# Kernel optimization log

Hardware: AMD Instinct MI355X
Metric: run time of the kernel (lower is better)

## Reference

```python
import jax, jax.numpy as jnp
import numpy as np

SAMPLING_RATE = 0.5

def setup_inputs() -> dict:
    key = jax.random.key(0)
    k1, k2 = jax.random.split(key)
    token = jax.random.normal(k1, (8, 16, 4, 384), dtype=jnp.float32)
    feature = jax.random.normal(k2, (8, 16, 4, 196, 384), dtype=jnp.float32)
    return {"token": token, "feature": feature}

def reference(token, feature):
    b1, n1, kk1, c = token.shape
    b2, n2, kk2, hw, _ = feature.shape
    N = n1 * kk1  # == n2 * kk2
    tok = token.reshape(b1, N, 1, c)           # [b, N, 1, c]
    feat = feature.reshape(b2, N, hw, c)       # [b, N, hw, c]
    scale = c ** (-0.5)
    # attention scores: [b, N, 1, hw]
    attn = jnp.einsum('bnqc,bnhc->bnqh', tok, feat) * scale
    attn = jax.nn.softmax(attn, axis=-1)
    tk = int(hw * SAMPLING_RATE)
    sel_attn, sel_idx = jax.lax.top_k(attn, tk)          # [b, N, 1, tk]
    sel_attn = sel_attn / jnp.sum(sel_attn, axis=-1, keepdims=True)
    # gather selected features: idx [b, N, tk] -> feat rows [b, N, tk, c]
    idx = sel_idx[:, :, 0, :]                            # [b, N, tk]
    sel_feat = jnp.take_along_axis(feat, idx[..., None], axis=2)  # [b, N, tk, c]
    out = jnp.einsum('bnqt,bntc->bnqc', sel_attn, sel_feat)       # [b, N, 1, c]
    return out.reshape(b1, n1, kk1, c)
```

## Files before the change

### kernel.cpp

```cpp
#include <hip/hip_runtime.h>
#include <hip/hip_fp16.h>

#define HW 196
#define C  384
#define CF4 (C/4)
#define TK 98
#define NT 512
#define NWAVE (NT/64)

__global__ __launch_bounds__(NT, 4) void sampling_kernel(
    const float* __restrict__ token,
    const float* __restrict__ feature,
    float* __restrict__ out)
{
    __shared__ __align__(16) unsigned char stash_raw[TK * C * 2];
    __shared__ float tokLds[C];
    __shared__ float score[HW];
    __shared__ float selW[TK];
    __shared__ int   selIdx[TK];
    __shared__ float wsum[NWAVE];
    __shared__ int   rank2[2 * HW];
    __shared__ float s_max, s_winv;

    __half (*feat16)[C] = (__half(*)[C])stash_raw;
    float  (*part)[C]   = (float(*)[C])stash_raw;

    const int tid  = threadIdx.x;
    const int wave = tid >> 6;
    const int lane = tid & 63;
    const int l8   = lane & 7;
    const int g8   = lane >> 3;
    const int pair = blockIdx.x;

    const float* tokp  = token   + (size_t)pair * C;
    const float* featp = feature + (size_t)pair * (HW * C);
    const float4* f4base = (const float4*)featp;
    const float4* t4     = (const float4*)tokLds;

    for (int i = tid; i < C; i += NT) tokLds[i] = tokp[i];
    __syncthreads();

    float4 tok[12];
    #pragma unroll
    for (int k = 0; k < 12; ++k) tok[k] = t4[l8 + 8 * k];

    const float scale = 0.05103103630798288f;

    #pragma unroll
    for (int it = 0; it < 3; ++it) {
        const int r = it * 64 + wave * 8 + g8;
        const float4* fr = f4base + (size_t)r * CF4 + l8;
        float4 a[12];
        #pragma unroll
        for (int k = 0; k < 12; ++k) a[k] = fr[8 * k];
        float4 acc = make_float4(0.f, 0.f, 0.f, 0.f);
        #pragma unroll
        for (int k = 0; k < 12; ++k) {
            acc.x += a[k].x * tok[k].x; acc.y += a[k].y * tok[k].y;
            acc.z += a[k].z * tok[k].z; acc.w += a[k].w * tok[k].w;
        }
        if (r < TK) {
            #pragma unroll
            for (int k = 0; k < 12; ++k) {
                union { uint2 u; __half2 h[2]; } W;
                W.h[0] = __floats2half2_rn(a[k].x, a[k].y);
                W.h[1] = __floats2half2_rn(a[k].z, a[k].w);
                *(uint2*)&feat16[r][4 * l8 + 32 * k] = W.u;
            }
        }
        float s = (acc.x + acc.y) + (acc.z + acc.w);
        s += __shfl_xor(s, 1, 64);
        s += __shfl_xor(s, 2, 64);
        s += __shfl_xor(s, 4, 64);
        if (l8 == 0) score[r] = s * scale;
    }
    if (wave < 4 && g8 == 0) {
        const int r = 192 + wave;
        const float4* fr = f4base + (size_t)r * CF4 + l8;
        float4 acc = make_float4(0.f, 0.f, 0.f, 0.f);
        #pragma unroll
        for (int k = 0; k < 12; ++k) {
            float4 a = fr[8 * k];
            acc.x += a.x * tok[k].x; acc.y += a.y * tok[k].y;
            acc.z += a.z * tok[k].z; acc.w += a.w * tok[k].w;
        }
        float s = (acc.x + acc.y) + (acc.z + acc.w);
        s += __shfl_xor(s, 1, 64);
        s += __shfl_xor(s, 2, 64);
        s += __shfl_xor(s, 4, 64);
        if (l8 == 0) score[r] = s * scale;
    }
    __syncthreads();

    if (tid < 2 * HW) {
        const int i = tid >> 1, h = tid & 1;
        const float si = score[i];
        int cnt = 0;
        const int j0 = h * (HW / 2);
        for (int j = j0; j < j0 + HW / 2; ++j) {
            const float sj = score[j];
            cnt += (int)((sj > si) | ((sj == si) & (j < i)));
        }
        rank2[tid] = cnt;
    } else if (wave == NWAVE - 1) {
        float m = -3.4e38f;
        for (int i = lane; i < HW; i += 64) m = fmaxf(m, score[i]);
        #pragma unroll
        for (int off = 32; off > 0; off >>= 1)
            m = fmaxf(m, __shfl_xor(m, off, 64));
        if (lane == 0) s_max = m;
    }
    __syncthreads();

    float w = 0.f;
    if (tid < HW) {
        const int rank = rank2[2 * tid] + rank2[2 * tid + 1];
        if (rank < TK) {
            w = __expf(score[tid] - s_max);
            selIdx[rank] = tid;
            selW[rank]  = w;
        }
    }
    #pragma unroll
    for (int off = 32; off > 0; off >>= 1) w += __shfl_xor(w, off, 64);
    if (lane == 0) wsum[wave] = w;
    __syncthreads();
    if (tid == 0) {
        float s = 0.f;
        #pragma unroll
        for (int i = 0; i < NWAVE; ++i) s += wsum[i];
        s_winv = 1.f / s;
    }
    __syncthreads();

    float4 acc_a = make_float4(0.f, 0.f, 0.f, 0.f);
    float4 acc_b = make_float4(0.f, 0.f, 0.f, 0.f);
    #pragma unroll
    for (int j = 0; j < 13; ++j) {
        const int i = wave + NWAVE * j;
        if (i < TK) {
            const int   r   = selIdx[i];
            const float wgt = selW[i];
            if (r < TK) {
                union { uint2 u; __half2 h[2]; } U;
                U.u = *(const uint2*)&feat16[r][4 * lane];
                float2 f0 = __half22float2(U.h[0]);
                float2 f1 = __half22float2(U.h[1]);
                acc_a.x += wgt * f0.x; acc_a.y += wgt * f0.y;
                acc_a.z += wgt * f1.x; acc_a.w += wgt * f1.y;
                if (lane < 32) {
                    union { uint2 u; __half2 h[2]; } V;
                    V.u = *(const uint2*)&feat16[r][256 + 4 * lane];
                    float2 g0 = __half22float2(V.h[0]);
                    float2 g1 = __half22float2(V.h[1]);
                    acc_b.x += wgt * g0.x; acc_b.y += wgt * g0.y;
                    acc_b.z += wgt * g1.x; acc_b.w += wgt * g1.y;
                }
            } else {
                const float4* f4 = f4base + (size_t)r * CF4;
                float4 aa = f4[lane];
                acc_a.x += wgt * aa.x; acc_a.y += wgt * aa.y;
                acc_a.z += wgt * aa.z; acc_a.w += wgt * aa.w;
                if (lane < 32) {
                    float4 bb = f4[64 + lane];
                    acc_b.x += wgt * bb.x; acc_b.y += wgt * bb.y;
                    acc_b.z += wgt * bb.z; acc_b.w += wgt * bb.w;
                }
            }
        }
    }
    __syncthreads();

    float4* pw = (float4*)&part[wave][0];
    pw[lane] = acc_a;
    if (lane < 32) pw[64 + lane] = acc_b;
    __syncthreads();

    if (tid < C) {
        float s = 0.f;
        #pragma unroll
        for (int wv = 0; wv < NWAVE; ++wv) s += part[wv][tid];
        out[(size_t)pair * C + tid] = s * s_winv;
    }
}

extern "C" void kernel_launch(void* const* d_in, const int* in_sizes, int n_in,
                              void* d_out, int out_size, void* d_ws, size_t ws_size,
                              hipStream_t stream) {
    const float* token   = (const float*)d_in[0];
    const float* feature = (const float*)d_in[1];
    float* out = (float*)d_out;
    const int pairs = in_sizes[0] / C;
    sampling_kernel<<<pairs, NT, 0, stream>>>(token, feature, out);
}
```

Baseline: 36.87 us.

## Keep first 128 feature rows in registers as fp16, stash rest in LDS

The kernel no longer re-reads unstashed selected rows from global memory. Rows 0-127 are now held in registers as fp16 and accumulated with per-row weights (zero when not selected) plus cross-lane shuffle reductions. The remaining 68 rows are stashed in LDS with a padded stride. This removes the second global gather for rows 98-195 and the separate top-k gather for low rows, at the cost of more registers, shuffle work and extra LDS (separate part buffer), which may reduce occupancy.

```diff
diff --git a/kernel.cpp b/kernel.cpp
--- a/kernel.cpp
+++ b/kernel.cpp
@@ -7,23 +7,24 @@
 #define TK 98
 #define NT 512
 #define NWAVE (NT/64)
+#define RSTRIDE 400
+#define NSTASH 68
 
 __global__ __launch_bounds__(NT, 4) void sampling_kernel(
     const float* __restrict__ token,
     const float* __restrict__ feature,
     float* __restrict__ out)
 {
-    __shared__ __align__(16) unsigned char stash_raw[TK * C * 2];
+    __shared__ __half stash[NSTASH * RSTRIDE];
     __shared__ float tokLds[C];
     __shared__ float score[HW];
+    __shared__ float wFlag[128];
     __shared__ float selW[TK];
     __shared__ int   selIdx[TK];
+    __shared__ int   rank2[2 * HW];
     __shared__ float wsum[NWAVE];
-    __shared__ int   rank2[2 * HW];
+    __shared__ float part[NWAVE][C];
     __shared__ float s_max, s_winv;
-
-    __half (*feat16)[C] = (__half(*)[C])stash_raw;
-    float  (*part)[C]   = (float(*)[C])stash_raw;
 
     const int tid  = threadIdx.x;
     const int wave = tid >> 6;
@@ -32,22 +33,19 @@
     const int g8   = lane >> 3;
     const int pair = blockIdx.x;
 
-    const float* tokp  = token   + (size_t)pair * C;
-    const float* featp = feature + (size_t)pair * (HW * C);
-    const float4* f4base = (const float4*)featp;
-    const float4* t4     = (const float4*)tokLds;
+    const float* tokp = token + (size_t)pair * C;
+    const float4* f4base = (const float4*)(feature + (size_t)pair * (HW * C));
+    const float4* t4 = (const float4*)tokLds;
 
     for (int i = tid; i < C; i += NT) tokLds[i] = tokp[i];
     __syncthreads();
 
-    float4 tok[12];
+    const float scale = 0.05103103630798288f;
+
+    uint2 r16[2][12];
+
     #pragma unroll
-    for (int k = 0; k < 12; ++k) tok[k] = t4[l8 + 8 * k];
-
-    const float scale = 0.05103103630798288f;
-
-    #pragma unroll
-    for (int it = 0; it < 3; ++it) {
+    for (int it = 0; it < 2; ++it) {
         const int r = it * 64 + wave * 8 + g8;
         const float4* fr = f4base + (size_t)r * CF4 + l8;
         float4 a[12];
@@ -56,17 +54,13 @@
         float4 acc = make_float4(0.f, 0.f, 0.f, 0.f);
         #pragma unroll
         for (int k = 0; k < 12; ++k) {
-            acc.x += a[k].x * tok[k].x; acc.y += a[k].y * tok[k].y;
-            acc.z += a[k].z * tok[k].z; acc.w += a[k].w * tok[k].w;
-        }
-        if (r < TK) {
-            #pragma unroll
-            for (int k = 0; k < 12; ++k) {
-                union { uint2 u; __half2 h[2]; } W;
-                W.h[0] = __floats2half2_rn(a[k].x, a[k].y);
-                W.h[1] = __floats2half2_rn(a[k].z, a[k].w);
-                *(uint2*)&feat16[r][4 * l8 + 32 * k] = W.u;
-            }
+            float4 t = t4[l8 + 8 * k];
+            acc.x += a[k].x * t.x; acc.y += a[k].y * t.y;
+            acc.z += a[k].z * t.z; acc.w += a[k].w * t.w;
+            union { uint2 u; __half2 h[2]; } W;
+            W.h[0] = __floats2half2_rn(a[k].x, a[k].y);
+            W.h[1] = __floats2half2_rn(a[k].z, a[k].w);
+            r16[it][k] = W.u;
         }
         float s = (acc.x + acc.y) + (acc.z + acc.w);
         s += __shfl_xor(s, 1, 64);
@@ -74,15 +68,46 @@
         s += __shfl_xor(s, 4, 64);
         if (l8 == 0) score[r] = s * scale;
     }
+
+    {
+        const int r = 128 + wave * 8 + g8;
+        const float4* fr = f4base + (size_t)r * CF4 + l8;
+        __half* srow = &stash[(r - 128) * RSTRIDE];
+        float4 a[12];
+        #pragma unroll
+        for (int k = 0; k < 12; ++k) a[k] = fr[8 * k];
+        float4 acc = make_float4(0.f, 0.f, 0.f, 0.f);
+        #pragma unroll
+        for (int k = 0; k < 12; ++k) {
+            float4 t = t4[l8 + 8 * k];
+            acc.x += a[k].x * t.x; acc.y += a[k].y * t.y;
+            acc.z += a[k].z * t.z; acc.w += a[k].w * t.w;
+            union { uint2 u; __half2 h[2]; } W;
+            W.h[0] = __floats2half2_rn(a[k].x, a[k].y);
+            W.h[1] = __floats2half2_rn(a[k].z, a[k].w);
+            *(uint2*)&srow[4 * l8 + 32 * k] = W.u;
+        }
+        float s = (acc.x + acc.y) + (acc.z + acc.w);
+        s += __shfl_xor(s, 1, 64);
+        s += __shfl_xor(s, 2, 64);
+        s += __shfl_xor(s, 4, 64);
+        if (l8 == 0) score[r] = s * scale;
+    }
     if (wave < 4 && g8 == 0) {
         const int r = 192 + wave;
         const float4* fr = f4base + (size_t)r * CF4 + l8;
+        __half* srow = &stash[(r - 128) * RSTRIDE];
         float4 acc = make_float4(0.f, 0.f, 0.f, 0.f);
         #pragma unroll
         for (int k = 0; k < 12; ++k) {
             float4 a = fr[8 * k];
-            acc.x += a.x * tok[k].x; acc.y += a.y * tok[k].y;
-            acc.z += a.z * tok[k].z; acc.w += a.w * tok[k].w;
+            float4 t = t4[l8 + 8 * k];
+            acc.x += a.x * t.x; acc.y += a.y * t.y;
+            acc.z += a.z * t.z; acc.w += a.w * t.w;
+            union { uint2 u; __half2 h[2]; } W;
+            W.h[0] = __floats2half2_rn(a.x, a.y);
+            W.h[1] = __floats2half2_rn(a.z, a.w);
+            *(uint2*)&srow[4 * l8 + 32 * k] = W.u;
         }
         float s = (acc.x + acc.y) + (acc.z + acc.w);
         s += __shfl_xor(s, 1, 64);
@@ -115,11 +140,14 @@
     float w = 0.f;
     if (tid < HW) {
         const int rank = rank2[2 * tid] + rank2[2 * tid + 1];
+        float wv = 0.f;
         if (rank < TK) {
-            w = __expf(score[tid] - s_max);
+            wv = __expf(score[tid] - s_max);
             selIdx[rank] = tid;
-            selW[rank]  = w;
-        }
+            selW[rank]  = wv;
+        }
+        if (tid < 128) wFlag[tid] = wv;
+        w = wv;
     }
     #pragma unroll
     for (int off = 32; off > 0; off >>= 1) w += __shfl_xor(w, off, 64);
@@ -130,6 +158,40 @@
         #pragma unroll
         for (int i = 0; i < NWAVE; ++i) s += wsum[i];
         s_winv = 1.f / s;
+    }
+    __syncthreads();
+
+    {
+        const int row0 = wave * 8 + g8;
+        const float w0 = wFlag[row0];
+        const float w1 = wFlag[64 + row0];
+        float4 av[12];
+        #pragma unroll
+        for (int k = 0; k < 12; ++k) {
+            union { uint2 u; __half2 h[2]; } A, B;
+            A.u = r16[0][k]; B.u = r16[1][k];
+            float2 a0 = __half22float2(A.h[0]), a1 = __half22float2(A.h[1]);
+            float2 b0 = __half22float2(B.h[0]), b1 = __half22float2(B.h[1]);
+            av[k].x = w0 * a0.x + w1 * b0.x;
+            av[k].y = w0 * a0.y + w1 * b0.y;
+            av[k].z = w0 * a1.x + w1 * b1.x;
+            av[k].w = w0 * a1.y + w1 * b1.y;
+        }
+        #pragma unroll
+        for (int lvl = 8; lvl <= 32; lvl <<= 1) {
+            #pragma unroll
+            for (int k = 0; k < 12; ++k) {
+                av[k].x += __shfl_xor(av[k].x, lvl, 64);
+                av[k].y += __shfl_xor(av[k].y, lvl, 64);
+                av[k].z += __shfl_xor(av[k].z, lvl, 64);
+                av[k].w += __shfl_xor(av[k].w, lvl, 64);
+            }
+        }
+        if (g8 == 0) {
+            #pragma unroll
+            for (int k = 0; k < 12; ++k)
+                *(float4*)&part[wave][4 * l8 + 32 * k] = av[k];
+        }
     }
     __syncthreads();
 
@@ -139,41 +201,38 @@
     for (int j = 0; j < 13; ++j) {
         const int i = wave + NWAVE * j;
         if (i < TK) {
-            const int   r   = selIdx[i];
-            const float wgt = selW[i];
-            if (r < TK) {
+            const int r = selIdx[i];
+            if (r >= 128) {
+                const float wgt = selW[i];
+                const __half* row = &stash[(r - 128) * RSTRIDE];
                 union { uint2 u; __half2 h[2]; } U;
-                U.u = *(const uint2*)&feat16[r][4 * lane];
+                U.u = *(const uint2*)&row[4 * lane];
                 float2 f0 = __half22float2(U.h[0]);
                 float2 f1 = __half22float2(U.h[1]);
                 acc_a.x += wgt * f0.x; acc_a.y += wgt * f0.y;
                 acc_a.z += wgt * f1.x; acc_a.w += wgt * f1.y;
                 if (lane < 32) {
                     union { uint2 u; __half2 h[2]; } V;
-                    V.u = *(const uint2*)&feat16[r][256 + 4 * lane];
+                    V.u = *(const uint2*)&row[256 + 4 * lane];
                     float2 g0 = __half22float2(V.h[0]);
                     float2 g1 = __half22float2(V.h[1]);
                     acc_b.x += wgt * g0.x; acc_b.y += wgt * g0.y;
                     acc_b.z += wgt * g1.x; acc_b.w += wgt * g1.y;
                 }
-            } else {
-                const float4* f4 = f4base + (size_t)r * CF4;
-                float4 aa = f4[lane];
-                acc_a.x += wgt * aa.x; acc_a.y += wgt * aa.y;
-                acc_a.z += wgt * aa.z; acc_a.w += wgt * aa.w;
-                if (lane < 32) {
-                    float4 bb = f4[64 + lane];
-                    acc_b.x += wgt * bb.x; acc_b.y += wgt * bb.y;
-                    acc_b.z += wgt * bb.z; acc_b.w += wgt * bb.w;
-                }
             }
         }
     }
-    __syncthreads();
-
-    float4* pw = (float4*)&part[wave][0];
-    pw[lane] = acc_a;
-    if (lane < 32) pw[64 + lane] = acc_b;
+    {
+        float4* pw = (float4*)&part[wave][0];
+        float4 cur = pw[lane];
+        cur.x += acc_a.x; cur.y += acc_a.y; cur.z += acc_a.z; cur.w += acc_a.w;
+        pw[lane] = cur;
+        if (lane < 32) {
+            float4 c2 = pw[64 + lane];
+            c2.x += acc_b.x; c2.y += acc_b.y; c2.z += acc_b.z; c2.w += acc_b.w;
+            pw[64 + lane] = c2;
+        }
+    }
     __syncthreads();
 
     if (tid < C) {
```

Result: slower. 56.29 us (+52.7%).
